# Optimization experiments

Measured on AMD Instinct MI355X. Metric: run time of the kernel, lower is better.

Reference implementation:

```python
import jax, jax.numpy as jnp
import numpy as np

BS = 512
N_BOXES = 30   # num_boxes*3 in the torch module
K = 15
HID = 128
EMB = 64
FEAT = HID + EMB + 2  # 194


def _knn_idx(x, k):
    # x: (bs, n, 4); per-sample kNN (self excluded), matching pyg knn_graph with batch
    d = jnp.sum((x[:, :, None, :] - x[:, None, :, :]) ** 2, axis=-1)  # (bs, n, n)
    n = x.shape[1]
    d = d + jnp.eye(n, dtype=x.dtype) * 1e9  # exclude self-loops
    _, idx = jax.lax.top_k(-d, k)  # k nearest sources j for each target i
    return idx  # (bs, n, k)


def _edge_conv(x, idx, Wa, ba, Wb, bb):
    # EdgeConv: out_i = max_j mlp([x_i, x_j - x_i]), aggr='max'
    xj = jax.vmap(lambda xb, ib: xb[ib])(x, idx)            # (bs, n, k, F)
    xi = jnp.broadcast_to(x[:, :, None, :], xj.shape)        # (bs, n, k, F)
    m = jnp.concatenate([xi, xj - xi], axis=-1)              # (bs, n, k, 2F)
    h = jax.nn.relu(jnp.einsum('bnkf,hf->bnkh', m, Wa) + ba)
    h = jnp.einsum('bnkh,oh->bnko', h, Wb) + bb
    return jnp.max(h, axis=2)                                # (bs, n, HID)


def _q(nodes, emb, Wi, bi, Wma, bma, Wmb, bmb, Wca, bca, Wcb, bcb):
    bs, n, _ = nodes.shape
    idx = _knn_idx(nodes, K)
    cats = jnp.repeat(jnp.arange(3), n // 3)                 # [0]*10+[1]*10+[2]*10
    cls = jax.nn.relu(emb[cats])                             # (n, EMB)
    cls = jnp.broadcast_to(cls[None], (bs, n, EMB))
    tar = jnp.zeros((bs, n, 2), nodes.dtype)                 # tanh(zeros) = 0
    init = jnp.concatenate([jax.nn.relu(nodes @ Wi.T + bi), cls, tar], axis=-1)
    h = jax.nn.relu(_edge_conv(init, idx, Wma, bma, Wmb, bmb))
    h = jax.nn.relu(h @ Wca.T + bca)
    out = h @ Wcb.T + bcb                                    # (bs, n, 1)
    return out.reshape(bs, -1)


def setup_inputs() -> dict:
    key = jax.random.key(0)
    ks = jax.random.split(key, 22)
    rn = lambda k, shp: (jax.random.normal(k, shp) * 0.05).astype(jnp.float32)
    return {
        'state': jax.random.normal(ks[0], (BS, N_BOXES * 2), jnp.float32),
        'action': jax.random.normal(ks[1], (BS, N_BOXES * 2), jnp.float32),
        'W_init1': rn(ks[2], (HID, 4)), 'b_init1': rn(ks[3], (HID,)),
        'emb1': rn(ks[4], (3, EMB)),
        'W_m1a': rn(ks[5], (HID, 2 * FEAT)), 'b_m1a': rn(ks[6], (HID,)),
        'W_m1b': rn(ks[7], (HID, HID)), 'b_m1b': rn(ks[8], (HID,)),
        'W_c1a': rn(ks[9], (HID, HID)), 'b_c1a': rn(ks[10], (HID,)),
        'W_c1b': rn(ks[11], (1, HID)), 'b_c1b': rn(ks[12], (1,)),
        'W_init2': rn(ks[13], (HID, 4)), 'b_init2': rn(ks[14], (HID,)),
        'emb2': rn(ks[15], (3, EMB)),
        'W_c2a': rn(ks[16], (HID, HID)), 'b_c2a': rn(ks[17], (HID,)),
        'W_c2b': rn(ks[18], (1, HID)), 'b_c2b': rn(ks[19], (1,)),
    }


def reference(state, action, W_init1, b_init1, emb1, W_m1a, b_m1a, W_m1b, b_m1b,
              W_c1a, b_c1a, W_c1b, b_c1b, W_init2, b_init2, emb2,
              W_c2a, b_c2a, W_c2b, b_c2b):
    bs = state.shape[0]
    # Q1 node layout: interleaved per-box [sx, sy, ax, ay]
    nodes1 = jnp.concatenate([state.reshape(bs, N_BOXES, 2),
                              action.reshape(bs, N_BOXES, 2)], axis=-1)
    q1 = _q(nodes1, emb1, W_init1, b_init1, W_m1a, b_m1a, W_m1b, b_m1b,
            W_c1a, b_c1a, W_c1b, b_c1b)
    # Q2 node layout (faithful to torch bug): cat along dim 1 then view(-1, 4)
    nodes2 = jnp.concatenate([state, action], axis=1).reshape(bs, N_BOXES, 4)
    # conv1_2 reuses mlp1_1 weights (faithful to torch source)
    q2 = _q(nodes2, emb2, W_init2, b_init2, W_m1a, b_m1a, W_m1b, b_m1b,
            W_c2a, b_c2a, W_c2b, b_c2b)
    return (q1, q2)
```

## Files before the change

### kernel.cpp

```cpp
#include <hip/hip_runtime.h>

#define BSZ 512
#define NNODE 30
#define KNBR 15
#define HID 128
#define MTOT (BSZ*NNODE)

typedef __attribute__((ext_vector_type(8))) __bf16 bf16x8;
typedef __attribute__((ext_vector_type(4))) float f32x4;

__device__ __forceinline__ float frelu(float x){ return x > 0.f ? x : 0.f; }

__device__ __forceinline__ void node_coords(const float* __restrict__ st,
                                            const float* __restrict__ ac,
                                            int b, int n, int qsel, float c[4]) {
    if (qsel == 0) {
        c[0] = st[b*60 + 2*n];     c[1] = st[b*60 + 2*n + 1];
        c[2] = ac[b*60 + 2*n];     c[3] = ac[b*60 + 2*n + 1];
    } else {
        int base = 4*n;
        if (base < 60) {
            c[0]=st[b*60+base]; c[1]=st[b*60+base+1]; c[2]=st[b*60+base+2]; c[3]=st[b*60+base+3];
        } else {
            int a = base - 60;
            c[0]=ac[b*60+a]; c[1]=ac[b*60+a+1]; c[2]=ac[b*60+a+2]; c[3]=ac[b*60+a+3];
        }
    }
}

__global__ void k_prep(const float* __restrict__ Wa,  const float* __restrict__ Wb,
                       const float* __restrict__ Wca1,const float* __restrict__ Wca2,
                       const float* __restrict__ ba,
                       const float* __restrict__ emb1,const float* __restrict__ emb2,
                       __bf16* __restrict__ Wc16, __bf16* __restrict__ Wb16,
                       __bf16* __restrict__ Wca16_1, __bf16* __restrict__ Wca16_2,
                       float* __restrict__ cls1A, float* __restrict__ cls1B,
                       float* __restrict__ cls2A, float* __restrict__ cls2B) {
    int blk = blockIdx.x;
    if (blk < 320) {
        int t = blk*256 + threadIdx.x;
        if (t < 32768) {
            int o = t >> 7, h = t & 127;
            float v = (o < 128) ? (Wa[o*388 + h] - Wa[o*388 + 194 + h])
                                : Wa[(o-128)*388 + 194 + h];
            Wc16[t] = (__bf16)v;
        } else if (t < 49152) { int u = t - 32768; Wb16[u]    = (__bf16)Wb[u]; }
        else if (t < 65536)   { int u = t - 49152; Wca16_1[u] = (__bf16)Wca1[u]; }
        else                  { int u = t - 65536; Wca16_2[u] = (__bf16)Wca2[u]; }
    } else {
        int o = threadIdx.x;
        if (o >= 128) return;
        const float* emb = (blk == 320) ? emb1  : emb2;
        float* cA        = (blk == 320) ? cls1A : cls2A;
        float* cB        = (blk == 320) ? cls1B : cls2B;
        for (int c = 0; c < 3; ++c) {
            float sA = ba[o], sB = 0.f;
            for (int e = 0; e < 64; ++e) {
                float r  = frelu(emb[c*64 + e]);
                float wl = Wa[o*388 + 128 + e];
                float wr = Wa[o*388 + 194 + 128 + e];
                sA += (wl - wr) * r;
                sB += wr * r;
            }
            cA[c*128 + o] = sA;
            cB[c*128 + o] = sB;
        }
    }
}

__global__ void __launch_bounds__(256) k_fused(
        const float* __restrict__ st, const float* __restrict__ ac, int qsel,
        const float* __restrict__ Wi, const float* __restrict__ bi,
        const __bf16* __restrict__ Wc16,
        const float* __restrict__ clsA, const float* __restrict__ clsB,
        const __bf16* __restrict__ Wb16, const float* __restrict__ bb,
        const __bf16* __restrict__ Wca16, const float* __restrict__ bca,
        const float* __restrict__ Wcb, const float* __restrict__ bcb,
        float* __restrict__ out, int qoff) {
    __shared__ float  coords[30][4];
    __shared__ int    idxs[30*16];
    __shared__ __bf16 Vf[2][4][4][16][8];
    __shared__ float  Al[30*132];
    __shared__ float  Bl[30*132];
    __shared__ __bf16 El[32*136];
    __shared__ float  redh[4][16];

    int tid  = threadIdx.x;
    int lane = tid & 63, wid = tid >> 6;
    int l15  = lane & 15, g = (lane >> 4) & 3;
    int b    = blockIdx.x;

    if (tid < 30) {
        float c[4]; node_coords(st, ac, b, tid, qsel, c);
        coords[tid][0]=c[0]; coords[tid][1]=c[1]; coords[tid][2]=c[2]; coords[tid][3]=c[3];
    }
    __syncthreads();

    if (tid < 30) {
        int i = tid;
        float ci0=coords[i][0], ci1=coords[i][1], ci2=coords[i][2], ci3=coords[i][3];
        float d[30];
        #pragma unroll
        for (int j = 0; j < 30; ++j) {
            float d0 = ci0-coords[j][0], d1 = ci1-coords[j][1];
            float d2 = ci2-coords[j][2], d3 = ci3-coords[j][3];
            d[j] = d0*d0 + d1*d1 + d2*d2 + d3*d3;
        }
        unsigned mask = 1u << i;
        for (int k = 0; k < KNBR; ++k) {
            float best = 3.4e38f; int bj = 0;
            #pragma unroll
            for (int j = 0; j < 30; ++j) {
                bool ok = !((mask >> j) & 1u) && (d[j] < best);
                if (ok) { best = d[j]; bj = j; }
            }
            mask |= 1u << bj;
            idxs[i*16 + k] = bj;
        }
        idxs[i*16 + 15] = idxs[i*16];
    } else if (tid >= 32) {
        for (int e = tid - 32; e < 4096; e += 224) {
            int m = e >> 7, h = e & 127;
            float v = 0.f;
            if (m < 30) {
                v = frelu(bi[h] + Wi[h*4+0]*coords[m][0] + Wi[h*4+1]*coords[m][1]
                                + Wi[h*4+2]*coords[m][2] + Wi[h*4+3]*coords[m][3]);
            }
            Vf[m>>4][h>>5][(h>>3)&3][m&15][h&7] = (__bf16)v;
        }
    }
    __syncthreads();

    {
        int mt = wid & 1, half = wid >> 1;
        bf16x8 af[4];
        #pragma unroll
        for (int kk = 0; kk < 4; ++kk) af[kk] = *(const bf16x8*)&Vf[mt][kk][g][l15][0];
        f32x4 acc[8];
        #pragma unroll
        for (int nc = 0; nc < 8; ++nc) acc[nc] = (f32x4){0.f,0.f,0.f,0.f};
        #pragma unroll
        for (int nc = 0; nc < 8; ++nc) {
            int o256 = half*128 + nc*16 + l15;
            bf16x8 wf[4];
            #pragma unroll
            for (int kk = 0; kk < 4; ++kk)
                wf[kk] = *(const bf16x8*)(Wc16 + o256*128 + kk*32 + g*8);
            #pragma unroll
            for (int kk = 0; kk < 4; ++kk)
                acc[nc] = __builtin_amdgcn_mfma_f32_16x16x32_bf16(af[kk], wf[kk], acc[nc], 0, 0, 0);
        }
        const float* cls = half ? clsB : clsA;
        float* dst = half ? Bl : Al;
        #pragma unroll
        for (int nc = 0; nc < 8; ++nc) {
            #pragma unroll
            for (int r = 0; r < 4; ++r) {
                int m = mt*16 + g*4 + r;
                if (m < 30) {
                    int o = nc*16 + l15;
                    int cat = m / 10;
                    dst[m*132 + o] = acc[nc][r] + cls[cat*128 + o];
                }
            }
        }
    }
    __syncthreads();

    {
        bf16x8 wbf[8][4];
        #pragma unroll
        for (int oc = 0; oc < 8; ++oc)
            #pragma unroll
            for (int kk = 0; kk < 4; ++kk)
                wbf[oc][kk] = *(const bf16x8*)(Wb16 + (oc*16 + l15)*128 + kk*32 + g*8);
        float bbv[8];
        #pragma unroll
        for (int oc = 0; oc < 8; ++oc) bbv[oc] = bb[oc*16 + l15];

        for (int i = wid; i < 30; i += 4) {
            int nb = idxs[i*16 + l15];
            bf16x8 hf[4];
            #pragma unroll
            for (int kk = 0; kk < 4; ++kk) {
                const float4* pa = (const float4*)&Al[i*132  + kk*32 + g*8];
                const float4* pb = (const float4*)&Bl[nb*132 + kk*32 + g*8];
                float4 a0 = pa[0], a1 = pa[1];
                float4 b0 = pb[0], b1 = pb[1];
                bf16x8 h;
                h[0]=(__bf16)frelu(a0.x+b0.x); h[1]=(__bf16)frelu(a0.y+b0.y);
                h[2]=(__bf16)frelu(a0.z+b0.z); h[3]=(__bf16)frelu(a0.w+b0.w);
                h[4]=(__bf16)frelu(a1.x+b1.x); h[5]=(__bf16)frelu(a1.y+b1.y);
                h[6]=(__bf16)frelu(a1.z+b1.z); h[7]=(__bf16)frelu(a1.w+b1.w);
                hf[kk] = h;
            }
            f32x4 acc[8];
            #pragma unroll
            for (int oc = 0; oc < 8; ++oc) acc[oc] = (f32x4){0.f,0.f,0.f,0.f};
            #pragma unroll
            for (int kk = 0; kk < 4; ++kk)
                #pragma unroll
                for (int oc = 0; oc < 8; ++oc)
                    acc[oc] = __builtin_amdgcn_mfma_f32_16x16x32_bf16(hf[kk], wbf[oc][kk], acc[oc], 0, 0, 0);
            #pragma unroll
            for (int oc = 0; oc < 8; ++oc) {
                float v = fmaxf(fmaxf(acc[oc][0], acc[oc][1]), fmaxf(acc[oc][2], acc[oc][3]));
                v = fmaxf(v, __shfl_xor(v, 16));
                v = fmaxf(v, __shfl_xor(v, 32));
                if (g == 0) El[i*136 + oc*16 + l15] = (__bf16)frelu(v + bbv[oc]);
            }
        }
        if (tid < 136) ((unsigned*)El)[2040 + tid] = 0u;
    }
    __syncthreads();

    {
        int mt = wid & 1, half = wid >> 1;
        bf16x8 ef[4];
        #pragma unroll
        for (int kk = 0; kk < 4; ++kk)
            ef[kk] = *(const bf16x8*)&El[(mt*16 + l15)*136 + kk*32 + g*8];
        float s[4] = {0.f, 0.f, 0.f, 0.f};
        #pragma unroll
        for (int nc = 0; nc < 4; ++nc) {
            int o = half*64 + nc*16 + l15;
            bf16x8 wf[4];
            #pragma unroll
            for (int kk = 0; kk < 4; ++kk)
                wf[kk] = *(const bf16x8*)(Wca16 + o*128 + kk*32 + g*8);
            f32x4 a = (f32x4){0.f,0.f,0.f,0.f};
            #pragma unroll
            for (int kk = 0; kk < 4; ++kk)
                a = __builtin_amdgcn_mfma_f32_16x16x32_bf16(ef[kk], wf[kk], a, 0, 0, 0);
            float bcav = bca[o], wcbv = Wcb[o];
            #pragma unroll
            for (int r = 0; r < 4; ++r) s[r] += frelu(a[r] + bcav) * wcbv;
        }
        #pragma unroll
        for (int r = 0; r < 4; ++r) {
            s[r] += __shfl_xor(s[r], 1);
            s[r] += __shfl_xor(s[r], 2);
            s[r] += __shfl_xor(s[r], 4);
            s[r] += __shfl_xor(s[r], 8);
        }
        if (l15 == 0) {
            #pragma unroll
            for (int r = 0; r < 4; ++r) redh[wid][g*4 + r] = s[r];
        }
    }
    __syncthreads();
    if (tid < 30) {
        int mt = tid >> 4, mr = tid & 15;
        out[qoff + b*30 + tid] = redh[mt][mr] + redh[mt+2][mr] + bcb[0];
    }
}

extern "C" void kernel_launch(void* const* d_in, const int* in_sizes, int n_in,
                              void* d_out, int out_size, void* d_ws, size_t ws_size,
                              hipStream_t stream) {
    const float* state  = (const float*)d_in[0];
    const float* action = (const float*)d_in[1];
    const float* W_init1= (const float*)d_in[2];
    const float* b_init1= (const float*)d_in[3];
    const float* emb1   = (const float*)d_in[4];
    const float* W_m1a  = (const float*)d_in[5];
    const float* b_m1a  = (const float*)d_in[6];
    const float* W_m1b  = (const float*)d_in[7];
    const float* b_m1b  = (const float*)d_in[8];
    const float* W_c1a  = (const float*)d_in[9];
    const float* b_c1a  = (const float*)d_in[10];
    const float* W_c1b  = (const float*)d_in[11];
    const float* b_c1b  = (const float*)d_in[12];
    const float* W_init2= (const float*)d_in[13];
    const float* b_init2= (const float*)d_in[14];
    const float* emb2   = (const float*)d_in[15];
    const float* W_c2a  = (const float*)d_in[16];
    const float* b_c2a  = (const float*)d_in[17];
    const float* W_c2b  = (const float*)d_in[18];
    const float* b_c2b  = (const float*)d_in[19];

    __bf16* Wc16    = (__bf16*)d_ws;
    __bf16* Wb16    = Wc16 + 32768;
    __bf16* Wca16_1 = Wb16 + 16384;
    __bf16* Wca16_2 = Wca16_1 + 16384;
    float*  cls1A   = (float*)(Wca16_2 + 16384);
    float*  cls1B   = cls1A + 384;
    float*  cls2A   = cls1B + 384;
    float*  cls2B   = cls2A + 384;
    float*  out     = (float*)d_out;

    k_prep<<<322, 256, 0, stream>>>(W_m1a, W_m1b, W_c1a, W_c2a, b_m1a, emb1, emb2,
                                    Wc16, Wb16, Wca16_1, Wca16_2,
                                    cls1A, cls1B, cls2A, cls2B);

    k_fused<<<BSZ, 256, 0, stream>>>(state, action, 0, W_init1, b_init1,
                                     Wc16, cls1A, cls1B, Wb16, b_m1b,
                                     Wca16_1, b_c1a, W_c1b, b_c1b, out, 0);
    k_fused<<<BSZ, 256, 0, stream>>>(state, action, 1, W_init2, b_init2,
                                     Wc16, cls2A, cls2B, Wb16, b_m1b,
                                     Wca16_2, b_c2a, W_c2b, b_c2b, out, MTOT);
}
```

Measured before the change: 197.7 us.

## Merge Q1/Q2 launches, store edge pre-activations in bf16, chunk output channels

Fuses the two per-Q kernel launches into a single grid of 1024 blocks that selects its weights by block index. The per-node A/B pre-activation buffers move from fp32 to bf16 in LDS, which roughly halves shared-memory use. The edge MLP second layer now runs in two output-channel chunks so only half of Wb is held in registers, and launch bounds ask for 4 blocks per CU. Together these aim to raise occupancy and drop a launch, at the cost of extra bf16 rounding before the ReLU add and of recomputing the edge features for each chunk.

```diff
diff --git a/kernel.cpp b/kernel.cpp
--- a/kernel.cpp
+++ b/kernel.cpp
@@ -68,30 +68,44 @@
     }
 }
 
-__global__ void __launch_bounds__(256) k_fused(
-        const float* __restrict__ st, const float* __restrict__ ac, int qsel,
-        const float* __restrict__ Wi, const float* __restrict__ bi,
+__global__ void __launch_bounds__(256, 4) k_fused(
+        const float* __restrict__ st, const float* __restrict__ ac,
+        const float* __restrict__ Wi1, const float* __restrict__ bi1,
+        const float* __restrict__ Wi2, const float* __restrict__ bi2,
         const __bf16* __restrict__ Wc16,
-        const float* __restrict__ clsA, const float* __restrict__ clsB,
+        const float* __restrict__ cls1A, const float* __restrict__ cls1B,
+        const float* __restrict__ cls2A, const float* __restrict__ cls2B,
         const __bf16* __restrict__ Wb16, const float* __restrict__ bb,
-        const __bf16* __restrict__ Wca16, const float* __restrict__ bca,
-        const float* __restrict__ Wcb, const float* __restrict__ bcb,
-        float* __restrict__ out, int qoff) {
+        const __bf16* __restrict__ Wca16_1, const float* __restrict__ bca1,
+        const float* __restrict__ Wcb1, const float* __restrict__ bcb1,
+        const __bf16* __restrict__ Wca16_2, const float* __restrict__ bca2,
+        const float* __restrict__ Wcb2, const float* __restrict__ bcb2,
+        float* __restrict__ out) {
     __shared__ float  coords[30][4];
     __shared__ int    idxs[30*16];
-    __shared__ __bf16 Vf[2][4][4][16][8];
-    __shared__ float  Al[30*132];
-    __shared__ float  Bl[30*132];
-    __shared__ __bf16 El[32*136];
+    __shared__ __align__(16) __bf16 Vf[2][4][4][16][8];
+    __shared__ __align__(16) __bf16 Al[30*136];
+    __shared__ __align__(16) __bf16 Bl[30*136];
+    __shared__ __align__(16) __bf16 El[32*136];
     __shared__ float  redh[4][16];
 
     int tid  = threadIdx.x;
     int lane = tid & 63, wid = tid >> 6;
     int l15  = lane & 15, g = (lane >> 4) & 3;
-    int b    = blockIdx.x;
+    int bid  = blockIdx.x;
+    int q    = bid >> 9, b = bid & 511;
+
+    const float* Wi   = q ? Wi2 : Wi1;
+    const float* bi   = q ? bi2 : bi1;
+    const float* clsA = q ? cls2A : cls1A;
+    const float* clsB = q ? cls2B : cls1B;
+    const __bf16* Wca16 = q ? Wca16_2 : Wca16_1;
+    const float* bca  = q ? bca2 : bca1;
+    const float* Wcb  = q ? Wcb2 : Wcb1;
+    const float* bcb  = q ? bcb2 : bcb1;
 
     if (tid < 30) {
-        float c[4]; node_coords(st, ac, b, tid, qsel, c);
+        float c[4]; node_coords(st, ac, b, tid, q, c);
         coords[tid][0]=c[0]; coords[tid][1]=c[1]; coords[tid][2]=c[2]; coords[tid][3]=c[3];
     }
     __syncthreads();
@@ -129,6 +143,7 @@
             Vf[m>>4][h>>5][(h>>3)&3][m&15][h&7] = (__bf16)v;
         }
     }
+    if (tid >= 30 && tid < 32) { }
     __syncthreads();
 
     {
@@ -151,7 +166,7 @@
                 acc[nc] = __builtin_amdgcn_mfma_f32_16x16x32_bf16(af[kk], wf[kk], acc[nc], 0, 0, 0);
         }
         const float* cls = half ? clsB : clsA;
-        float* dst = half ? Bl : Al;
+        __bf16* dst = half ? Bl : Al;
         #pragma unroll
         for (int nc = 0; nc < 8; ++nc) {
             #pragma unroll
@@ -160,7 +175,7 @@
                 if (m < 30) {
                     int o = nc*16 + l15;
                     int cat = m / 10;
-                    dst[m*132 + o] = acc[nc][r] + cls[cat*128 + o];
+                    dst[m*136 + o] = (__bf16)(acc[nc][r] + cls[cat*128 + o]);
                 }
             }
         }
@@ -168,46 +183,45 @@
     __syncthreads();
 
     {
-        bf16x8 wbf[8][4];
-        #pragma unroll
-        for (int oc = 0; oc < 8; ++oc)
-            #pragma unroll
-            for (int kk = 0; kk < 4; ++kk)
-                wbf[oc][kk] = *(const bf16x8*)(Wb16 + (oc*16 + l15)*128 + kk*32 + g*8);
-        float bbv[8];
-        #pragma unroll
-        for (int oc = 0; oc < 8; ++oc) bbv[oc] = bb[oc*16 + l15];
-
-        for (int i = wid; i < 30; i += 4) {
-            int nb = idxs[i*16 + l15];
-            bf16x8 hf[4];
-            #pragma unroll
-            for (int kk = 0; kk < 4; ++kk) {
-                const float4* pa = (const float4*)&Al[i*132  + kk*32 + g*8];
-                const float4* pb = (const float4*)&Bl[nb*132 + kk*32 + g*8];
-                float4 a0 = pa[0], a1 = pa[1];
-                float4 b0 = pb[0], b1 = pb[1];
-                bf16x8 h;
-                h[0]=(__bf16)frelu(a0.x+b0.x); h[1]=(__bf16)frelu(a0.y+b0.y);
-                h[2]=(__bf16)frelu(a0.z+b0.z); h[3]=(__bf16)frelu(a0.w+b0.w);
-                h[4]=(__bf16)frelu(a1.x+b1.x); h[5]=(__bf16)frelu(a1.y+b1.y);
-                h[6]=(__bf16)frelu(a1.z+b1.z); h[7]=(__bf16)frelu(a1.w+b1.w);
-                hf[kk] = h;
-            }
-            f32x4 acc[8];
-            #pragma unroll
-            for (int oc = 0; oc < 8; ++oc) acc[oc] = (f32x4){0.f,0.f,0.f,0.f};
-            #pragma unroll
-            for (int kk = 0; kk < 4; ++kk)
-                #pragma unroll
-                for (int oc = 0; oc < 8; ++oc)
-                    acc[oc] = __builtin_amdgcn_mfma_f32_16x16x32_bf16(hf[kk], wbf[oc][kk], acc[oc], 0, 0, 0);
-            #pragma unroll
-            for (int oc = 0; oc < 8; ++oc) {
-                float v = fmaxf(fmaxf(acc[oc][0], acc[oc][1]), fmaxf(acc[oc][2], acc[oc][3]));
-                v = fmaxf(v, __shfl_xor(v, 16));
-                v = fmaxf(v, __shfl_xor(v, 32));
-                if (g == 0) El[i*136 + oc*16 + l15] = (__bf16)frelu(v + bbv[oc]);
+        for (int ch = 0; ch < 2; ++ch) {
+            bf16x8 wbf[4][4];
+            #pragma unroll
+            for (int oc = 0; oc < 4; ++oc)
+                #pragma unroll
+                for (int kk = 0; kk < 4; ++kk)
+                    wbf[oc][kk] = *(const bf16x8*)(Wb16 + ((ch*4+oc)*16 + l15)*128 + kk*32 + g*8);
+            float bbv[4];
+            #pragma unroll
+            for (int oc = 0; oc < 4; ++oc) bbv[oc] = bb[(ch*4+oc)*16 + l15];
+
+            for (int i = wid; i < 30; i += 4) {
+                int nb = idxs[i*16 + l15];
+                bf16x8 hf[4];
+                #pragma unroll
+                for (int kk = 0; kk < 4; ++kk) {
+                    bf16x8 pa = *(const bf16x8*)&Al[i*136  + kk*32 + g*8];
+                    bf16x8 pb = *(const bf16x8*)&Bl[nb*136 + kk*32 + g*8];
+                    bf16x8 h;
+                    #pragma unroll
+                    for (int e = 0; e < 8; ++e)
+                        h[e] = (__bf16)frelu((float)pa[e] + (float)pb[e]);
+                    hf[kk] = h;
+                }
+                f32x4 acc[4];
+                #pragma unroll
+                for (int oc = 0; oc < 4; ++oc) acc[oc] = (f32x4){0.f,0.f,0.f,0.f};
+                #pragma unroll
+                for (int kk = 0; kk < 4; ++kk)
+                    #pragma unroll
+                    for (int oc = 0; oc < 4; ++oc)
+                        acc[oc] = __builtin_amdgcn_mfma_f32_16x16x32_bf16(hf[kk], wbf[oc][kk], acc[oc], 0, 0, 0);
+                #pragma unroll
+                for (int oc = 0; oc < 4; ++oc) {
+                    float v = fmaxf(fmaxf(acc[oc][0], acc[oc][1]), fmaxf(acc[oc][2], acc[oc][3]));
+                    v = fmaxf(v, __shfl_xor(v, 16));
+                    v = fmaxf(v, __shfl_xor(v, 32));
+                    if (g == 0) El[i*136 + (ch*4+oc)*16 + l15] = (__bf16)frelu(v + bbv[oc]);
+                }
             }
         }
         if (tid < 136) ((unsigned*)El)[2040 + tid] = 0u;
@@ -251,7 +265,7 @@
     __syncthreads();
     if (tid < 30) {
         int mt = tid >> 4, mr = tid & 15;
-        out[qoff + b*30 + tid] = redh[mt][mr] + redh[mt+2][mr] + bcb[0];
+        out[q*MTOT + b*30 + tid] = redh[mt][mr] + redh[mt+2][mr] + bcb[0];
     }
 }
 
@@ -293,10 +307,11 @@
                                     Wc16, Wb16, Wca16_1, Wca16_2,
                                     cls1A, cls1B, cls2A, cls2B);
 
-    k_fused<<<BSZ, 256, 0, stream>>>(state, action, 0, W_init1, b_init1,
-                                     Wc16, cls1A, cls1B, Wb16, b_m1b,
-                                     Wca16_1, b_c1a, W_c1b, b_c1b, out, 0);
-    k_fused<<<BSZ, 256, 0, stream>>>(state, action, 1, W_init2, b_init2,
-                                     Wc16, cls2A, cls2B, Wb16, b_m1b,
-                                     Wca16_2, b_c2a, W_c2b, b_c2b, out, MTOT);
+    k_fused<<<2*BSZ, 256, 0, stream>>>(state, action,
+                                       W_init1, b_init1, W_init2, b_init2,
+                                       Wc16, cls1A, cls1B, cls2A, cls2B,
+                                       Wb16, b_m1b,
+                                       Wca16_1, b_c1a, W_c1b, b_c1b,
+                                       Wca16_2, b_c2a, W_c2b, b_c2b,
+                                       out);
 }
```

Result: faster. 173.7 us (-12.2%).
